# Optimization experiments

Hardware: AMD Instinct MI355X
Metric: run time of the kernel (lower is better)

Reference implementation:

```python
import jax, jax.numpy as jnp
import numpy as np

K = 3  # deform kernel size; stride = K//2 = 1, pad = K%2 = 1


def _conv3x3(x, w, b):
    y = jax.lax.conv_general_dilated(x, w, (1, 1), [(1, 1), (1, 1)],
                                     dimension_numbers=('NCHW', 'OIHW', 'NCHW'))
    return y + b[None, :, None, None]


def _channel_attention(x, w1, b1, w2, b2):
    # RCAN channel attention: GAP -> 1x1 conv -> ReLU -> 1x1 conv -> sigmoid -> scale
    y = jnp.mean(x, axis=(2, 3))                 # [N, C]
    y = jax.nn.relu(y @ w1.T + b1)               # [N, C//16]
    y = jax.nn.sigmoid(y @ w2.T + b2)            # [N, C]
    return x * y[:, :, None, None]


def _bilinear_gather(x, py, px):
    # x: [N,C,H,W]; py/px: [N,Ho,Wo] float sampling coords; zero padding outside.
    H, W = x.shape[2], x.shape[3]
    y0 = jnp.floor(py); x0 = jnp.floor(px)
    wy1 = py - y0; wx1 = px - x0
    wy0 = 1.0 - wy1; wx0 = 1.0 - wx1

    def corner(yi, xi):
        valid = (yi >= 0) & (yi <= H - 1) & (xi >= 0) & (xi <= W - 1)
        yc = jnp.clip(yi, 0, H - 1).astype(jnp.int32)
        xc = jnp.clip(xi, 0, W - 1).astype(jnp.int32)
        g = jax.vmap(lambda xb, yb, xb2: xb[:, yb, xb2])(x, yc, xc)  # [N,C,Ho,Wo]
        return g * valid[:, None, :, :].astype(x.dtype)

    return (corner(y0, x0) * (wy0 * wx0)[:, None]
            + corner(y0, x0 + 1.0) * (wy0 * wx1)[:, None]
            + corner(y0 + 1.0, x0) * (wy1 * wx0)[:, None]
            + corner(y0 + 1.0, x0 + 1.0) * (wy1 * wx1)[:, None])


def _deform_conv(x, offset, w, b, k=K, stride=1, pad=1):
    # torchvision deform_conv2d, offset_groups=1, no modulation mask.
    N, C, H, W = x.shape
    Ho = (H + 2 * pad - k) // stride + 1
    Wo = (W + 2 * pad - k) // stride + 1
    base_y = (jnp.arange(Ho) * stride - pad).astype(x.dtype)
    base_x = (jnp.arange(Wo) * stride - pad).astype(x.dtype)
    acc = jnp.zeros((N, w.shape[0], Ho, Wo), x.dtype)
    for i in range(k):
        for j in range(k):
            idx = i * k + j
            # torchvision layout: channel 2*idx is dy, 2*idx+1 is dx
            py = base_y[None, :, None] + i + offset[:, 2 * idx]
            px = base_x[None, None, :] + j + offset[:, 2 * idx + 1]
            sampled = _bilinear_gather(x, py, px)          # [N,C,Ho,Wo]
            acc = acc + jnp.einsum('nchw,oc->nohw', sampled, w[:, :, i, j])
    return acc + b[None, :, None, None]


def setup_inputs() -> dict:
    key = jax.random.key(0)
    ks = jax.random.split(key, 24)
    N, Cin, H, W = 8, 64, 192, 192
    Cout, sq = 64, Cin // 16
    s = 0.05
    inp = {
        'x': jax.random.normal(ks[0], (N, Cin, H, W), jnp.float32),
        'ref_x': jax.random.normal(ks[1], (N, 3, H, W), jnp.float32),
        'ref_w': jax.random.normal(ks[2], (Cin, 12, 3, 3), jnp.float32) * s,
        'ref_b': jnp.zeros((Cin,), jnp.float32),
        'off_w1': jax.random.normal(ks[3], (Cin, 2 * Cin, 3, 3), jnp.float32) * s,
        'off_b1': jnp.zeros((Cin,), jnp.float32),
        'ca1_w1': jax.random.normal(ks[4], (sq, Cin), jnp.float32) * s,
        'ca1_b1': jnp.zeros((sq,), jnp.float32),
        'ca1_w2': jax.random.normal(ks[5], (Cin, sq), jnp.float32) * s,
        'ca1_b2': jnp.zeros((Cin,), jnp.float32),
        'off_w2': jax.random.normal(ks[6], (Cin, Cin, 3, 3), jnp.float32) * s,
        'off_b2': jnp.zeros((Cin,), jnp.float32),
        'ca2_w1': jax.random.normal(ks[7], (sq, Cin), jnp.float32) * s,
        'ca2_b1': jnp.zeros((sq,), jnp.float32),
        'ca2_w2': jax.random.normal(ks[8], (Cin, sq), jnp.float32) * s,
        'ca2_b2': jnp.zeros((Cin,), jnp.float32),
        'off_w3': jax.random.normal(ks[9], (2 * K * K, Cin, 3, 3), jnp.float32) * 0.01,
        'off_b3': jnp.zeros((2 * K * K,), jnp.float32),
        'dcn_w': jax.random.normal(ks[10], (Cout, Cin, K, K), jnp.float32) * s,
        'dcn_b': jnp.zeros((Cout,), jnp.float32),
        'rgb_w': jax.random.normal(ks[11], (3, Cout, 3, 3), jnp.float32) * s,
        'rgb_b': jnp.zeros((3,), jnp.float32),
    }
    return inp


def reference(x, ref_x, ref_w, ref_b, off_w1, off_b1, ca1_w1, ca1_b1, ca1_w2, ca1_b2,
              off_w2, off_b2, ca2_w1, ca2_b1, ca2_w2, ca2_b2, off_w3, off_b3,
              dcn_w, dcn_b, rgb_w, rgb_b):
    # ref branch: 4-fold flip augmentation concat -> conv -> relu
    ref_cat = jnp.concatenate([ref_x, jnp.flip(ref_x, 2), jnp.flip(ref_x, 3),
                               jnp.flip(ref_x, (2, 3))], axis=1)
    ref_f = jax.nn.relu(_conv3x3(ref_cat, ref_w, ref_b))
    # offset branch
    t = jnp.concatenate([x, ref_f], axis=1)
    t = jax.nn.relu(_conv3x3(t, off_w1, off_b1))
    t = _channel_attention(t, ca1_w1, ca1_b1, ca1_w2, ca1_b2)
    t = jax.nn.relu(_conv3x3(t, off_w2, off_b2))
    t = _channel_attention(t, ca2_w1, ca2_b1, ca2_w2, ca2_b2)
    offset = _conv3x3(t, off_w3, off_b3)        # [N, 2*K*K, H, W]
    mask = offset
    xo = jax.nn.relu(_deform_conv(x, offset, dcn_w, dcn_b))
    rgb = _conv3x3(xo, rgb_w, rgb_b)
    return (xo, rgb, mask, offset)
```

## Files before the change

### kernel.cpp

```cpp
#include <hip/hip_runtime.h>
#include <hip/hip_bf16.h>
#include <math.h>

#define HH 192
#define WW 192
#define HW (192*192)

typedef __attribute__((ext_vector_type(8))) short bfrag;
typedef __attribute__((ext_vector_type(4))) float ffrag;

__device__ __forceinline__ float bf2f(ushort u){
    union { unsigned int i; float f; } c; c.i = ((unsigned int)u) << 16; return c.f;
}
__device__ __forceinline__ ushort f2bf(float f){
    __hip_bfloat16 h = __float2bfloat16(f);
    return *reinterpret_cast<ushort*>(&h);
}

__global__ __launch_bounds__(256)
void k_prep(const float* __restrict__ x, const float* __restrict__ rx,
            ushort* __restrict__ xbf, ushort* __restrict__ rcbf){
    const int n = blockIdx.y;
    const int tid = threadIdx.x;
    if (blockIdx.z == 0){
        __shared__ ushort sT[256*64];
        const int px0 = blockIdx.x * 256;
        for (int c = 0; c < 64; ++c){
            float v = x[((size_t)(n*64 + c))*HW + px0 + tid];
            int slot = (((c >> 3) ^ (tid & 7)) << 3) + (c & 7);
            sT[tid*64 + slot] = f2bf(v);
        }
        __syncthreads();
        for (int r = 0; r < 8; ++r){
            int u = r*256 + tid;
            int pl = u >> 3, g = u & 7;
            uint4 v = *(const uint4*)&sT[pl*64 + ((g ^ (pl & 7)) << 3)];
            *(uint4*)(xbf + ((size_t)n*HW + px0 + pl)*64 + g*8) = v;
        }
    } else {
        const int px = blockIdx.x*256 + tid;
        const int y = px / WW, xx = px - y*WW;
        ushort v[32];
#pragma unroll
        for (int m = 0; m < 4; ++m){
            int ry = (m & 1) ? (HH-1-y) : y;
            int rxp = (m & 2) ? (WW-1-xx) : xx;
#pragma unroll
            for (int c = 0; c < 3; ++c)
                v[m*3+c] = f2bf(rx[((size_t)(n*3+c))*HW + ry*WW + rxp]);
        }
#pragma unroll
        for (int j = 12; j < 32; ++j) v[j] = 0;
#pragma unroll
        for (int k = 0; k < 4; ++k)
            *(uint4*)(rcbf + ((size_t)n*HW + px)*32 + k*8) = *(uint4*)&v[k*8];
    }
}

__global__ void k_wfrag_all(const float* __restrict__ w0, const float* __restrict__ w1,
                            const float* __restrict__ w2, const float* __restrict__ w3,
                            const float* __restrict__ w4, const float* __restrict__ w5,
                            ushort* __restrict__ f0, ushort* __restrict__ f1,
                            ushort* __restrict__ f2, ushort* __restrict__ f3,
                            ushort* __restrict__ f4, ushort* __restrict__ f5){
    const float* w; ushort* wf; int cin_real, ncb, cout_real, mt;
    switch (blockIdx.y){
        case 0: w=w0; wf=f0; cin_real=12;  ncb=1; cout_real=64; mt=4; break;
        case 1: w=w1; wf=f1; cin_real=128; ncb=4; cout_real=64; mt=4; break;
        case 2: w=w2; wf=f2; cin_real=64;  ncb=2; cout_real=64; mt=4; break;
        case 3: w=w3; wf=f3; cin_real=64;  ncb=2; cout_real=18; mt=2; break;
        case 4: w=w4; wf=f4; cin_real=64;  ncb=2; cout_real=64; mt=4; break;
        default:w=w5; wf=f5; cin_real=64;  ncb=2; cout_real=3;  mt=1; break;
    }
    int idx = blockIdx.x*256 + threadIdx.x;
    int total = ncb*9*mt*512;
    if (idx >= total) return;
    int e = idx & 7;
    int lane = (idx >> 3) & 63;
    int rest = idx >> 9;
    int mtl = rest % mt;
    int tap = (rest / mt) % 9;
    int cb  = rest / (mt*9);
    int cout = mtl*16 + (lane & 15);
    int cin  = cb*32 + ((lane >> 4) << 3) + e;
    float v = 0.f;
    if (cout < cout_real && cin < cin_real)
        v = w[((size_t)cout*cin_real + cin)*9 + tap];
    wf[idx] = f2bf(v);
}

template<int NCB, int MT, bool SCALE, bool CONCAT, bool RELU, int OM, bool GAPP>
__device__ __forceinline__
void conv_body(const ushort* __restrict__ in0, const ushort* __restrict__ in1,
               const ushort* __restrict__ wf, const float* __restrict__ bias,
               const float* __restrict__ scale,
               ushort* __restrict__ obf, float* __restrict__ of0, float* __restrict__ of1,
               float* __restrict__ part, int cout_real)
{
    __shared__ ushort sXt[18*18*32];
    __shared__ float sG[4][4][16];
    const int tid = threadIdx.x;
    const int lane = tid & 63;
    const int wv = tid >> 6;
    const int n = blockIdx.z;
    const int ty0 = blockIdx.y*16, tx0 = blockIdx.x*16;
    const int lx = lane & 15;
    const int lg = lane >> 4;

    ffrag acc[MT][4];
#pragma unroll
    for (int mt = 0; mt < MT; ++mt)
#pragma unroll
        for (int q = 0; q < 4; ++q) acc[mt][q] = (ffrag){0.f,0.f,0.f,0.f};

    for (int cb = 0; cb < NCB; ++cb){
        __syncthreads();
        for (int u = tid; u < 1296; u += 256){
            int yy = u / 72; int rr = u - yy*72; int xx = rr >> 2; int g = rr & 3;
            int gy = ty0 - 1 + yy, gx = tx0 - 1 + xx;
            uint4 val = make_uint4(0,0,0,0);
            if (gy >= 0 && gy < HH && gx >= 0 && gx < WW){
                const ushort* src; int ch; int stride;
                if constexpr (CONCAT){
                    src = (cb < 2) ? in0 : in1;
                    ch = (cb & 1)*32 + g*8;
                    stride = 64;
                } else {
                    src = in0; ch = cb*32 + g*8; stride = NCB*32;
                }
                val = *(const uint4*)(src + ((size_t)n*HW + gy*WW + gx)*stride + ch);
                if constexpr (SCALE){
                    ushort* e = (ushort*)&val;
                    int cb8 = cb*32 + g*8;
#pragma unroll
                    for (int j = 0; j < 8; ++j)
                        e[j] = f2bf(bf2f(e[j]) * scale[n*64 + cb8 + j]);
                }
            }
            *(uint4*)&sXt[((yy*18 + xx)*4 + (g ^ ((xx >> 1) & 3)))*8] = val;
        }
        __syncthreads();

        const bfrag* wbase = (const bfrag*)wf + (size_t)cb*9*MT*64 + lane;
        bfrag a[MT];
#pragma unroll
        for (int mt = 0; mt < MT; ++mt) a[mt] = wbase[mt*64];

#pragma unroll
        for (int tap = 0; tap < 9; ++tap){
            const int ky = tap / 3, kx = tap % 3;
            bfrag an[MT];
            if (tap < 8){
#pragma unroll
                for (int mt = 0; mt < MT; ++mt) an[mt] = wbase[(tap+1)*MT*64 + mt*64];
            }
#pragma unroll
            for (int q = 0; q < 4; ++q){
                const int yl = wv*4 + q + ky;
                const int xl = lx + kx;
                bfrag b = *(const bfrag*)&sXt[((yl*18 + xl)*4 + (lg ^ ((xl >> 1) & 3)))*8];
#pragma unroll
                for (int mt = 0; mt < MT; ++mt)
                    acc[mt][q] = __builtin_amdgcn_mfma_f32_16x16x32_bf16(a[mt], b, acc[mt][q], 0, 0, 0);
            }
            if (tap < 8){
#pragma unroll
                for (int mt = 0; mt < MT; ++mt) a[mt] = an[mt];
            }
        }
    }
    const int gx = tx0 + lx;
    float psum[MT][4];
    if constexpr (GAPP){
#pragma unroll
        for (int mt = 0; mt < MT; ++mt)
#pragma unroll
            for (int j = 0; j < 4; ++j) psum[mt][j] = 0.f;
    }
#pragma unroll
    for (int mt = 0; mt < MT; ++mt){
        const int co0 = mt*16 + lg*4;
#pragma unroll
        for (int q = 0; q < 4; ++q){
            const int gy = ty0 + wv*4 + q;
            float r[4];
#pragma unroll
            for (int j = 0; j < 4; ++j){
                float bv = (co0 + j < cout_real) ? bias[co0 + j] : 0.f;
                float v = acc[mt][q][j] + bv;
                if (RELU) v = fmaxf(v, 0.f);
                r[j] = v;
            }
            if constexpr (GAPP){
#pragma unroll
                for (int j = 0; j < 4; ++j) psum[mt][j] += r[j];
            }
            if constexpr (OM & 1){
                ushort pk[4];
#pragma unroll
                for (int j = 0; j < 4; ++j) pk[j] = f2bf(r[j]);
                *(uint2*)(obf + ((size_t)n*HW + gy*WW + gx)*64 + co0) = *(uint2*)pk;
            }
            if constexpr (OM & 2){
#pragma unroll
                for (int j = 0; j < 4; ++j){
                    int c = co0 + j;
                    if (c < cout_real){
                        size_t o = ((size_t)(n*cout_real + c))*HW + (size_t)gy*WW + gx;
                        of0[o] = r[j];
                        if (of1) of1[o] = r[j];
                    }
                }
            }
        }
    }
    if constexpr (GAPP){
#pragma unroll
        for (int mt = 0; mt < MT; ++mt)
#pragma unroll
            for (int j = 0; j < 4; ++j){
                float v = psum[mt][j];
#pragma unroll
                for (int d = 1; d < 16; d <<= 1) v += __shfl_xor(v, d, 64);
                if (lx == 0) sG[wv][lg][mt*4 + j] = v;
            }
        __syncthreads();
        if (tid < 64){
            int mt = tid >> 4, lgc = (tid >> 2) & 3, j = tid & 3;
            float s = sG[0][lgc][mt*4+j] + sG[1][lgc][mt*4+j]
                    + sG[2][lgc][mt*4+j] + sG[3][lgc][mt*4+j];
            part[(((size_t)n*144) + blockIdx.y*12 + blockIdx.x)*64 + tid] = s;
        }
    }
}

__global__ __launch_bounds__(256, 2)
void kc_ref(const ushort* __restrict__ in0, const ushort* __restrict__ wf,
            const float* __restrict__ bias, ushort* __restrict__ obf){
    conv_body<1,4,false,false,true,1,false>(in0, nullptr, wf, bias, nullptr, obf, nullptr, nullptr, nullptr, 64);
}
__global__ __launch_bounds__(256, 2)
void kc_off1(const ushort* __restrict__ in0, const ushort* __restrict__ in1,
             const ushort* __restrict__ wf, const float* __restrict__ bias,
             ushort* __restrict__ obf, float* __restrict__ part){
    conv_body<4,4,false,true,true,1,true>(in0, in1, wf, bias, nullptr, obf, nullptr, nullptr, part, 64);
}
__global__ __launch_bounds__(256, 2)
void kc_off2(const ushort* __restrict__ in0, const ushort* __restrict__ wf,
             const float* __restrict__ bias, const float* __restrict__ scale,
             ushort* __restrict__ obf, float* __restrict__ part){
    conv_body<2,4,true,false,true,1,true>(in0, nullptr, wf, bias, scale, obf, nullptr, nullptr, part, 64);
}
__global__ __launch_bounds__(256, 2)
void kc_off3(const ushort* __restrict__ in0, const ushort* __restrict__ wf,
             const float* __restrict__ bias, const float* __restrict__ scale,
             float* __restrict__ of0, float* __restrict__ of1){
    conv_body<2,2,true,false,false,2,false>(in0, nullptr, wf, bias, scale, nullptr, of0, of1, nullptr, 18);
}
__global__ __launch_bounds__(256, 2)
void kc_rgb(const ushort* __restrict__ in0, const ushort* __restrict__ wf,
            const float* __restrict__ bias, float* __restrict__ of0){
    conv_body<2,1,false,false,false,2,false>(in0, nullptr, wf, bias, nullptr, nullptr, of0, nullptr, nullptr, 3);
}

__global__ void k_cafc(const float* __restrict__ part, const float* __restrict__ w1,
                       const float* __restrict__ b1, const float* __restrict__ w2,
                       const float* __restrict__ b2, float* __restrict__ s)
{
    int n = blockIdx.x;
    int c = threadIdx.x;
    __shared__ float y[64], z[4];
    float acc = 0.f;
    for (int b = 0; b < 144; ++b) acc += part[((size_t)n*144 + b)*64 + c];
    y[c] = acc * (1.f/(float)HW);
    __syncthreads();
    if (c < 4){
        float a = b1[c];
        for (int i = 0; i < 64; ++i) a = fmaf(w1[c*64+i], y[i], a);
        z[c] = fmaxf(a, 0.f);
    }
    __syncthreads();
    float a = b2[c];
#pragma unroll
    for (int q = 0; q < 4; ++q) a = fmaf(w2[c*4+q], z[q], a);
    s[n*64+c] = 1.f/(1.f+expf(-a));
}

__global__ __launch_bounds__(256, 2)
void k_dcnm(const ushort* __restrict__ xbf, const float* __restrict__ off,
            const ushort* __restrict__ wf, const float* __restrict__ bias,
            float* __restrict__ xo, ushort* __restrict__ xobf)
{
    __shared__ ushort sS[2][128*64];
    const int tid = threadIdx.x;
    const int lane = tid & 63;
    const int wv = tid >> 6;
    const int n = blockIdx.z;
    const int ty0 = blockIdx.y*8, tx0 = blockIdx.x*16;
    const int lx = lane & 15;
    const int lg = lane >> 4;
    const int gx_out = tx0 + lx;
    const int gp = tid >> 2;
    const int gg = tid & 3;

    const ushort* xn = xbf + (size_t)n*HW*64;
    const float* offn = off + (size_t)n*18*HW;

    ffrag acc[4][2];
#pragma unroll
    for (int mt = 0; mt < 4; ++mt)
#pragma unroll
        for (int q = 0; q < 2; ++q) acc[mt][q] = (ffrag){0.f,0.f,0.f,0.f};

    int buf = 0;
    for (int tap = 0; tap < 9; ++tap){
        const int ti = tap/3, tj = tap%3;
#pragma unroll
        for (int pass = 0; pass < 2; ++pass){
            const int p = pass*64 + gp;
            const int py_ = ty0 + (p >> 4), px_ = tx0 + (p & 15);
            float dy = offn[(size_t)(2*tap)*HW + py_*WW + px_];
            float dx = offn[(size_t)(2*tap+1)*HW + py_*WW + px_];
            float sy = (float)(py_ + ti - 1) + dy;
            float sx = (float)(px_ + tj - 1) + dx;
            float y0f = floorf(sy), x0f = floorf(sx);
            float wy1 = sy - y0f, wx1 = sx - x0f;
            float wy0 = 1.f - wy1, wx0 = 1.f - wx1;
            int y0 = (int)y0f, x0 = (int)x0f;
            int y1 = y0+1, x1 = x0+1;
            float vy0 = (y0 >= 0 && y0 < HH) ? 1.f : 0.f;
            float vy1 = (y1 >= 0 && y1 < HH) ? 1.f : 0.f;
            float vx0 = (x0 >= 0 && x0 < WW) ? 1.f : 0.f;
            float vx1 = (x1 >= 0 && x1 < WW) ? 1.f : 0.f;
            float w00 = wy0*wx0*vy0*vx0, w01 = wy0*wx1*vy0*vx1;
            float w10 = wy1*wx0*vy1*vx0, w11 = wy1*wx1*vy1*vx1;
            int yc0 = min(max(y0,0),HH-1), yc1 = min(max(y1,0),HH-1);
            int xc0 = min(max(x0,0),WW-1), xc1 = min(max(x1,0),WW-1);
            int b00 = (yc0*WW + xc0)*64, b01 = (yc0*WW + xc1)*64;
            int b10 = (yc1*WW + xc0)*64, b11 = (yc1*WW + xc1)*64;
#pragma unroll
            for (int cb = 0; cb < 2; ++cb){
                const int ch = cb*32 + gg*8;
                uint4 c00 = *(const uint4*)(xn + b00 + ch);
                uint4 c01 = *(const uint4*)(xn + b01 + ch);
                uint4 c10 = *(const uint4*)(xn + b10 + ch);
                uint4 c11 = *(const uint4*)(xn + b11 + ch);
                const ushort* e00 = (const ushort*)&c00;
                const ushort* e01 = (const ushort*)&c01;
                const ushort* e10 = (const ushort*)&c10;
                const ushort* e11 = (const ushort*)&c11;
                ushort pk[8];
#pragma unroll
                for (int j = 0; j < 8; ++j){
                    float s = bf2f(e00[j])*w00 + bf2f(e01[j])*w01
                            + bf2f(e10[j])*w10 + bf2f(e11[j])*w11;
                    pk[j] = f2bf(s);
                }
                const int sl = (cb*4 + gg) ^ (p & 7);
                *(uint4*)&sS[buf][p*64 + sl*8] = *(uint4*)pk;
            }
        }
        __syncthreads();
#pragma unroll
        for (int cb = 0; cb < 2; ++cb){
            const bfrag* wbase = (const bfrag*)wf + ((size_t)(cb*9 + tap)*4)*64 + lane;
            bfrag a[4];
#pragma unroll
            for (int mt = 0; mt < 4; ++mt) a[mt] = wbase[mt*64];
#pragma unroll
            for (int q = 0; q < 2; ++q){
                const int p = (wv*2 + q)*16 + lx;
                const int sl = (cb*4 + lg) ^ (p & 7);
                bfrag b = *(const bfrag*)&sS[buf][p*64 + sl*8];
#pragma unroll
                for (int mt = 0; mt < 4; ++mt)
                    acc[mt][q] = __builtin_amdgcn_mfma_f32_16x16x32_bf16(a[mt], b, acc[mt][q], 0, 0, 0);
            }
        }
        buf ^= 1;
    }
#pragma unroll
    for (int mt = 0; mt < 4; ++mt){
        const int co0 = mt*16 + lg*4;
#pragma unroll
        for (int q = 0; q < 2; ++q){
            const int gy = ty0 + wv*2 + q;
            float r[4];
            ushort pk[4];
#pragma unroll
            for (int j = 0; j < 4; ++j){
                r[j] = fmaxf(acc[mt][q][j] + bias[co0+j], 0.f);
                pk[j] = f2bf(r[j]);
            }
#pragma unroll
            for (int j = 0; j < 4; ++j)
                xo[((size_t)(n*64 + co0 + j))*HW + (size_t)gy*WW + gx_out] = r[j];
            *(uint2*)(xobf + ((size_t)n*HW + gy*WW + gx_out)*64 + co0) = *(uint2*)pk;
        }
    }
}

extern "C" void kernel_launch(void* const* d_in, const int* in_sizes, int n_in,
                              void* d_out, int out_size, void* d_ws, size_t ws_size,
                              hipStream_t stream)
{
    const float* x      = (const float*)d_in[0];
    const float* ref_x  = (const float*)d_in[1];
    const float* ref_w  = (const float*)d_in[2];
    const float* ref_b  = (const float*)d_in[3];
    const float* off_w1 = (const float*)d_in[4];
    const float* off_b1 = (const float*)d_in[5];
    const float* ca1_w1 = (const float*)d_in[6];
    const float* ca1_b1 = (const float*)d_in[7];
    const float* ca1_w2 = (const float*)d_in[8];
    const float* ca1_b2 = (const float*)d_in[9];
    const float* off_w2 = (const float*)d_in[10];
    const float* off_b2 = (const float*)d_in[11];
    const float* ca2_w1 = (const float*)d_in[12];
    const float* ca2_b1 = (const float*)d_in[13];
    const float* ca2_w2 = (const float*)d_in[14];
    const float* ca2_b2 = (const float*)d_in[15];
    const float* off_w3 = (const float*)d_in[16];
    const float* off_b3 = (const float*)d_in[17];
    const float* dcn_w  = (const float*)d_in[18];
    const float* dcn_b  = (const float*)d_in[19];
    const float* rgb_w  = (const float*)d_in[20];
    const float* rgb_b  = (const float*)d_in[21];

    float* out = (float*)d_out;
    const size_t XO  = (size_t)8 * 64 * HW;
    const size_t RGB = (size_t)8 * 3 * HW;
    const size_t OFF = (size_t)8 * 18 * HW;
    float* xo_out   = out;
    float* rgb_out  = out + XO;
    float* mask_out = out + XO + RGB;
    float* off_out  = out + XO + RGB + OFF;

    const size_t NPX = (size_t)8 * HW;
    ushort* ws16  = (ushort*)d_ws;
    ushort* x_bf  = ws16;
    ushort* bufP  = x_bf + NPX*64;
    ushort* bufQ  = bufP + NPX*64;
    ushort* rc_bf = bufQ + NPX*64;
    ushort* wf_ref = rc_bf + NPX*32;
    ushort* wf_1   = wf_ref + 18432;
    ushort* wf_2   = wf_1 + 73728;
    ushort* wf_3   = wf_2 + 36864;
    ushort* wf_d   = wf_3 + 18432;
    ushort* wf_r   = wf_d + 36864;
    float*  part1  = (float*)(wf_r + 9216);
    float*  part2  = part1 + 73728;
    float*  s1     = part2 + 73728;
    float*  s2     = s1 + 512;

    dim3 pg(144, 8, 2), cg(12, 12, 8), dg(12, 24, 8);

    k_prep<<<pg, 256, 0, stream>>>(x, ref_x, x_bf, rc_bf);
    k_wfrag_all<<<dim3(288, 6), 256, 0, stream>>>(
        ref_w, off_w1, off_w2, off_w3, dcn_w, rgb_w,
        wf_ref, wf_1, wf_2, wf_3, wf_d, wf_r);

    kc_ref<<<cg, 256, 0, stream>>>(rc_bf, wf_ref, ref_b, bufP);
    kc_off1<<<cg, 256, 0, stream>>>(x_bf, bufP, wf_1, off_b1, bufQ, part1);
    k_cafc<<<8, 64, 0, stream>>>(part1, ca1_w1, ca1_b1, ca1_w2, ca1_b2, s1);
    kc_off2<<<cg, 256, 0, stream>>>(bufQ, wf_2, off_b2, s1, bufP, part2);
    k_cafc<<<8, 64, 0, stream>>>(part2, ca2_w1, ca2_b1, ca2_w2, ca2_b2, s2);
    kc_off3<<<cg, 256, 0, stream>>>(bufP, wf_3, off_b3, s2, off_out, mask_out);
    k_dcnm<<<dg, 256, 0, stream>>>(x_bf, off_out, wf_d, dcn_b, xo_out, bufQ);
    kc_rgb<<<cg, 256, 0, stream>>>(bufQ, wf_r, rgb_b, rgb_out);
}
```

Baseline: 333.2 us.

## Stage 64-channel input tiles in LDS to halve conv barrier rounds

```diff
diff --git a/kernel.cpp b/kernel.cpp
--- a/kernel.cpp
+++ b/kernel.cpp
@@ -91,13 +91,102 @@
 
 template<int NCB, int MT, bool SCALE, bool CONCAT, bool RELU, int OM, bool GAPP>
 __device__ __forceinline__
-void conv_body(const ushort* __restrict__ in0, const ushort* __restrict__ in1,
-               const ushort* __restrict__ wf, const float* __restrict__ bias,
-               const float* __restrict__ scale,
-               ushort* __restrict__ obf, float* __restrict__ of0, float* __restrict__ of1,
-               float* __restrict__ part, int cout_real)
+void conv_body32(const ushort* __restrict__ in0, const ushort* __restrict__ in1,
+                 const ushort* __restrict__ wf, const float* __restrict__ bias,
+                 const float* __restrict__ scale,
+                 ushort* __restrict__ obf, float* __restrict__ of0, float* __restrict__ of1,
+                 float* __restrict__ part, int cout_real)
 {
     __shared__ ushort sXt[18*18*32];
+    const int tid = threadIdx.x;
+    const int lane = tid & 63;
+    const int wv = tid >> 6;
+    const int n = blockIdx.z;
+    const int ty0 = blockIdx.y*16, tx0 = blockIdx.x*16;
+    const int lx = lane & 15;
+    const int lg = lane >> 4;
+
+    ffrag acc[MT][4];
+#pragma unroll
+    for (int mt = 0; mt < MT; ++mt)
+#pragma unroll
+        for (int q = 0; q < 4; ++q) acc[mt][q] = (ffrag){0.f,0.f,0.f,0.f};
+
+    for (int cb = 0; cb < NCB; ++cb){
+        __syncthreads();
+        for (int u = tid; u < 1296; u += 256){
+            int yy = u / 72; int rr = u - yy*72; int xx = rr >> 2; int g = rr & 3;
+            int gy = ty0 - 1 + yy, gx = tx0 - 1 + xx;
+            uint4 val = make_uint4(0,0,0,0);
+            if (gy >= 0 && gy < HH && gx >= 0 && gx < WW){
+                val = *(const uint4*)(in0 + ((size_t)n*HW + gy*WW + gx)*(NCB*32) + cb*32 + g*8);
+            }
+            *(uint4*)&sXt[((yy*18 + xx)*4 + (g ^ ((xx >> 1) & 3)))*8] = val;
+        }
+        __syncthreads();
+
+        const bfrag* wbase = (const bfrag*)wf + (size_t)cb*9*MT*64 + lane;
+        bfrag a[MT];
+#pragma unroll
+        for (int mt = 0; mt < MT; ++mt) a[mt] = wbase[mt*64];
+
+#pragma unroll
+        for (int tap = 0; tap < 9; ++tap){
+            const int ky = tap / 3, kx = tap % 3;
+            bfrag an[MT];
+            if (tap < 8){
+#pragma unroll
+                for (int mt = 0; mt < MT; ++mt) an[mt] = wbase[(tap+1)*MT*64 + mt*64];
+            }
+#pragma unroll
+            for (int q = 0; q < 4; ++q){
+                const int yl = wv*4 + q + ky;
+                const int xl = lx + kx;
+                bfrag b = *(const bfrag*)&sXt[((yl*18 + xl)*4 + (lg ^ ((xl >> 1) & 3)))*8];
+#pragma unroll
+                for (int mt = 0; mt < MT; ++mt)
+                    acc[mt][q] = __builtin_amdgcn_mfma_f32_16x16x32_bf16(a[mt], b, acc[mt][q], 0, 0, 0);
+            }
+            if (tap < 8){
+#pragma unroll
+                for (int mt = 0; mt < MT; ++mt) a[mt] = an[mt];
+            }
+        }
+    }
+    const int gx = tx0 + lx;
+#pragma unroll
+    for (int mt = 0; mt < MT; ++mt){
+        const int co0 = mt*16 + lg*4;
+#pragma unroll
+        for (int q = 0; q < 4; ++q){
+            const int gy = ty0 + wv*4 + q;
+            float r[4];
+#pragma unroll
+            for (int j = 0; j < 4; ++j){
+                float bv = (co0 + j < cout_real) ? bias[co0 + j] : 0.f;
+                float v = acc[mt][q][j] + bv;
+                if (RELU) v = fmaxf(v, 0.f);
+                r[j] = v;
+            }
+            if constexpr (OM & 1){
+                ushort pk[4];
+#pragma unroll
+                for (int j = 0; j < 4; ++j) pk[j] = f2bf(r[j]);
+                *(uint2*)(obf + ((size_t)n*HW + gy*WW + gx)*64 + co0) = *(uint2*)pk;
+            }
+        }
+    }
+}
+
+template<int NC64, int MT, bool SCALE, bool CONCAT, bool RELU, int OM, bool GAPP>
+__device__ __forceinline__
+void conv_body64(const ushort* __restrict__ in0, const ushort* __restrict__ in1,
+                 const ushort* __restrict__ wf, const float* __restrict__ bias,
+                 const float* __restrict__ scale,
+                 ushort* __restrict__ obf, float* __restrict__ of0, float* __restrict__ of1,
+                 float* __restrict__ part, int cout_real)
+{
+    __shared__ ushort sXt[18*18*64];
     __shared__ float sG[4][4][16];
     const int tid = threadIdx.x;
     const int lane = tid & 63;
@@ -113,59 +202,59 @@
 #pragma unroll
         for (int q = 0; q < 4; ++q) acc[mt][q] = (ffrag){0.f,0.f,0.f,0.f};
 
-    for (int cb = 0; cb < NCB; ++cb){
-        __syncthreads();
-        for (int u = tid; u < 1296; u += 256){
-            int yy = u / 72; int rr = u - yy*72; int xx = rr >> 2; int g = rr & 3;
+    for (int c64 = 0; c64 < NC64; ++c64){
+        if (c64) __syncthreads();
+        for (int u = tid; u < 2592; u += 256){
+            int g = u & 7;
+            int pix = u >> 3;
+            int yy = pix / 18, xx = pix - yy*18;
             int gy = ty0 - 1 + yy, gx = tx0 - 1 + xx;
             uint4 val = make_uint4(0,0,0,0);
             if (gy >= 0 && gy < HH && gx >= 0 && gx < WW){
-                const ushort* src; int ch; int stride;
-                if constexpr (CONCAT){
-                    src = (cb < 2) ? in0 : in1;
-                    ch = (cb & 1)*32 + g*8;
-                    stride = 64;
-                } else {
-                    src = in0; ch = cb*32 + g*8; stride = NCB*32;
-                }
-                val = *(const uint4*)(src + ((size_t)n*HW + gy*WW + gx)*stride + ch);
+                const ushort* src;
+                if constexpr (CONCAT) src = (c64 == 0) ? in0 : in1;
+                else src = in0;
+                val = *(const uint4*)(src + ((size_t)n*HW + gy*WW + gx)*64 + g*8);
                 if constexpr (SCALE){
                     ushort* e = (ushort*)&val;
-                    int cb8 = cb*32 + g*8;
 #pragma unroll
                     for (int j = 0; j < 8; ++j)
-                        e[j] = f2bf(bf2f(e[j]) * scale[n*64 + cb8 + j]);
+                        e[j] = f2bf(bf2f(e[j]) * scale[n*64 + g*8 + j]);
                 }
             }
-            *(uint4*)&sXt[((yy*18 + xx)*4 + (g ^ ((xx >> 1) & 3)))*8] = val;
+            *(uint4*)&sXt[(pix*8 + (g ^ (xx & 7)))*8] = val;
         }
         __syncthreads();
 
-        const bfrag* wbase = (const bfrag*)wf + (size_t)cb*9*MT*64 + lane;
-        bfrag a[MT];
-#pragma unroll
-        for (int mt = 0; mt < MT; ++mt) a[mt] = wbase[mt*64];
-
-#pragma unroll
-        for (int tap = 0; tap < 9; ++tap){
-            const int ky = tap / 3, kx = tap % 3;
-            bfrag an[MT];
-            if (tap < 8){
-#pragma unroll
-                for (int mt = 0; mt < MT; ++mt) an[mt] = wbase[(tap+1)*MT*64 + mt*64];
-            }
-#pragma unroll
-            for (int q = 0; q < 4; ++q){
-                const int yl = wv*4 + q + ky;
-                const int xl = lx + kx;
-                bfrag b = *(const bfrag*)&sXt[((yl*18 + xl)*4 + (lg ^ ((xl >> 1) & 3)))*8];
-#pragma unroll
-                for (int mt = 0; mt < MT; ++mt)
-                    acc[mt][q] = __builtin_amdgcn_mfma_f32_16x16x32_bf16(a[mt], b, acc[mt][q], 0, 0, 0);
-            }
-            if (tap < 8){
-#pragma unroll
-                for (int mt = 0; mt < MT; ++mt) a[mt] = an[mt];
+#pragma unroll
+        for (int sub = 0; sub < 2; ++sub){
+            const int cb = c64*2 + sub;
+            const bfrag* wbase = (const bfrag*)wf + (size_t)cb*9*MT*64 + lane;
+            bfrag a[MT];
+#pragma unroll
+            for (int mt = 0; mt < MT; ++mt) a[mt] = wbase[mt*64];
+#pragma unroll
+            for (int tap = 0; tap < 9; ++tap){
+                const int ky = tap / 3, kx = tap % 3;
+                bfrag an[MT];
+                if (tap < 8){
+#pragma unroll
+                    for (int mt = 0; mt < MT; ++mt) an[mt] = wbase[(tap+1)*MT*64 + mt*64];
+                }
+#pragma unroll
+                for (int q = 0; q < 4; ++q){
+                    const int yl = wv*4 + q + ky;
+                    const int xl = lx + kx;
+                    const int gi = sub*4 + lg;
+                    bfrag b = *(const bfrag*)&sXt[(((yl*18 + xl)*8) + (gi ^ (xl & 7)))*8];
+#pragma unroll
+                    for (int mt = 0; mt < MT; ++mt)
+                        acc[mt][q] = __builtin_amdgcn_mfma_f32_16x16x32_bf16(a[mt], b, acc[mt][q], 0, 0, 0);
+                }
+                if (tap < 8){
+#pragma unroll
+                    for (int mt = 0; mt < MT; ++mt) a[mt] = an[mt];
+                }
             }
         }
     }
@@ -237,30 +326,30 @@
 __global__ __launch_bounds__(256, 2)
 void kc_ref(const ushort* __restrict__ in0, const ushort* __restrict__ wf,
             const float* __restrict__ bias, ushort* __restrict__ obf){
-    conv_body<1,4,false,false,true,1,false>(in0, nullptr, wf, bias, nullptr, obf, nullptr, nullptr, nullptr, 64);
+    conv_body32<1,4,false,false,true,1,false>(in0, nullptr, wf, bias, nullptr, obf, nullptr, nullptr, nullptr, 64);
 }
 __global__ __launch_bounds__(256, 2)
 void kc_off1(const ushort* __restrict__ in0, const ushort* __restrict__ in1,
              const ushort* __restrict__ wf, const float* __restrict__ bias,
              ushort* __restrict__ obf, float* __restrict__ part){
-    conv_body<4,4,false,true,true,1,true>(in0, in1, wf, bias, nullptr, obf, nullptr, nullptr, part, 64);
+    conv_body64<2,4,false,true,true,1,true>(in0, in1, wf, bias, nullptr, obf, nullptr, nullptr, part, 64);
 }
 __global__ __launch_bounds__(256, 2)
 void kc_off2(const ushort* __restrict__ in0, const ushort* __restrict__ wf,
              const float* __restrict__ bias, const float* __restrict__ scale,
              ushort* __restrict__ obf, float* __restrict__ part){
-    conv_body<2,4,true,false,true,1,true>(in0, nullptr, wf, bias, scale, obf, nullptr, nullptr, part, 64);
+    conv_body64<1,4,true,false,true,1,true>(in0, nullptr, wf, bias, scale, obf, nullptr, nullptr, part, 64);
 }
 __global__ __launch_bounds__(256, 2)
 void kc_off3(const ushort* __restrict__ in0, const ushort* __restrict__ wf,
              const float* __restrict__ bias, const float* __restrict__ scale,
              float* __restrict__ of0, float* __restrict__ of1){
-    conv_body<2,2,true,false,false,2,false>(in0, nullptr, wf, bias, scale, nullptr, of0, of1, nullptr, 18);
+    conv_body64<1,2,true,false,false,2,false>(in0, nullptr, wf, bias, scale, nullptr, of0, of1, nullptr, 18);
 }
 __global__ __launch_bounds__(256, 2)
 void kc_rgb(const ushort* __restrict__ in0, const ushort* __restrict__ wf,
             const float* __restrict__ bias, float* __restrict__ of0){
-    conv_body<2,1,false,false,false,2,false>(in0, nullptr, wf, bias, nullptr, nullptr, of0, nullptr, nullptr, 3);
+    conv_body64<1,1,false,false,false,2,false>(in0, nullptr, wf, bias, nullptr, nullptr, of0, nullptr, nullptr, 3);
 }
 
 __global__ void k_cafc(const float* __restrict__ part, const float* __restrict__ w1,
```

New measurement: 338.4 us. No clear change (+1.6%).
